# Optimization experiments

Measured on AMD Instinct MI355X. Metric: run time of the kernel, lower is better.

Reference implementation:

```python
import jax, jax.numpy as jnp
import numpy as np

N_NODES = 50000
N_EDGES = 1600000
N_GRAPHS = 64


def gcn_conv(x, edge_index, W, b):
    """GCNConv: out = D^{-1/2} (A + I) D^{-1/2} X W + b (symmetric norm, self-loops)."""
    n = x.shape[0]
    src = jnp.concatenate([edge_index[0], jnp.arange(n)])  # add self-loops
    dst = jnp.concatenate([edge_index[1], jnp.arange(n)])
    deg = jax.ops.segment_sum(jnp.ones_like(dst, dtype=x.dtype), dst, num_segments=n)
    dinv = jax.lax.rsqrt(jnp.maximum(deg, 1.0))
    norm = dinv[src] * dinv[dst]                      # [E+N]
    h = x @ W                                          # transform first (smaller gather)
    msg = norm[:, None] * h[src]                       # [E+N, out_dim]
    out = jax.ops.segment_sum(msg, dst, num_segments=n)
    return out + b


def global_mean_pool(x, batch, num_graphs):
    s = jax.ops.segment_sum(x, batch, num_segments=num_graphs)
    cnt = jax.ops.segment_sum(jnp.ones((x.shape[0],), x.dtype), batch, num_segments=num_graphs)
    return s / jnp.maximum(cnt, 1.0)[:, None]


def setup_inputs() -> dict:
    key = jax.random.key(0)
    ks = jax.random.split(key, 6)
    x = jax.random.normal(ks[0], (N_NODES, 256), dtype=jnp.float32)
    edge_index = jax.random.randint(ks[1], (2, N_EDGES), 0, N_NODES, dtype=jnp.int64)
    batch = jnp.sort(jax.random.randint(ks[2], (N_NODES,), 0, N_GRAPHS, dtype=jnp.int64))
    W1 = jax.random.normal(ks[3], (256, 256), dtype=jnp.float32) * (1.0 / np.sqrt(256))
    b1 = jnp.zeros((256,), jnp.float32)
    W2 = jax.random.normal(ks[4], (256, 10), dtype=jnp.float32) * (1.0 / np.sqrt(256))
    b2 = jnp.zeros((10,), jnp.float32)
    return {"x": x, "edge_index": edge_index, "batch": batch,
            "W1": W1, "b1": b1, "W2": W2, "b2": b2}


def reference(x, edge_index, batch, W1, b1, W2, b2):
    h = gcn_conv(x, edge_index, W1, b1)
    h = jax.nn.elu(h)
    # dropout: identity (inference mode, training=False)
    h = gcn_conv(h, edge_index, W2, b2)
    h = jax.nn.elu(h)
    g = global_mean_pool(h, batch, N_GRAPHS)          # [num_graphs, num_class]
    return jax.nn.log_softmax(g, axis=-1)
```

## Files before the change

kernel.cpp:

```cpp
#include <hip/hip_runtime.h>
#include <hip/hip_bf16.h>
#include <math.h>

typedef unsigned int uint;
typedef unsigned short ushort;

typedef __attribute__((ext_vector_type(8))) short bf16x8;
typedef __attribute__((ext_vector_type(4))) float f32x4;

#define SBLK_SHIFT 12
#define SBLK_STRIDE 16

__device__ __forceinline__ float bf2f_lo(uint u) {
    return __uint_as_float(u << 16);
}
__device__ __forceinline__ float bf2f_hi(uint u) {
    return __uint_as_float(u & 0xffff0000u);
}
__device__ __forceinline__ ushort f2bf(float f) {
    uint u = __float_as_uint(f);
    uint rounding = 0x7fffu + ((u >> 16) & 1u);
    return (ushort)((u + rounding) >> 16);
}
__device__ __forceinline__ float elu(float x) {
    return x > 0.f ? x : expm1f(x);
}

__global__ void count2_kernel(const int* __restrict__ src, const int* __restrict__ dst, int E,
                              int* __restrict__ cnt2) {
    int i = blockIdx.x * blockDim.x + threadIdx.x;
    int stride = gridDim.x * blockDim.x;
    for (; i < E; i += stride)
        atomicAdd(&cnt2[dst[i] * SBLK_STRIDE + (src[i] >> SBLK_SHIFT)], 1);
}

__global__ void scan1_kernel(const int* __restrict__ cnt, int M, int* __restrict__ partials) {
    __shared__ int sh[256];
    int i = blockIdx.x * 256 + threadIdx.x;
    sh[threadIdx.x] = (i < M) ? cnt[i] : 0;
    __syncthreads();
    for (int s = 128; s > 0; s >>= 1) {
        if (threadIdx.x < s) sh[threadIdx.x] += sh[threadIdx.x + s];
        __syncthreads();
    }
    if (threadIdx.x == 0) partials[blockIdx.x] = sh[0];
}

__global__ __launch_bounds__(256) void scan2_kernel(const int* __restrict__ partials, int nb,
                                                    int* __restrict__ pscan) {
    __shared__ int tsum[256];
    int t = threadIdx.x;
    int pref[16];
    int s = 0;
    #pragma unroll
    for (int j = 0; j < 16; ++j) {
        int idx = t * 16 + j;
        int v = (idx < nb) ? partials[idx] : 0;
        pref[j] = s;
        s += v;
    }
    tsum[t] = s;
    __syncthreads();
    for (int d = 1; d < 256; d <<= 1) {
        int x = (t >= d) ? tsum[t - d] : 0;
        __syncthreads();
        tsum[t] += x;
        __syncthreads();
    }
    int base = (t == 0) ? 0 : tsum[t - 1];
    #pragma unroll
    for (int j = 0; j < 16; ++j) {
        int idx = t * 16 + j;
        if (idx < nb) pscan[idx] = base + pref[j];
    }
}

__global__ void scan3_kernel(const int* __restrict__ cnt, int M, const int* __restrict__ pscan,
                             int* __restrict__ offs2, int* __restrict__ cursor2) {
    __shared__ int sh[256];
    int t = threadIdx.x;
    int i = blockIdx.x * 256 + t;
    int v = (i < M) ? cnt[i] : 0;
    sh[t] = v;
    __syncthreads();
    for (int d = 1; d < 256; d <<= 1) {
        int x = (t >= d) ? sh[t - d] : 0;
        __syncthreads();
        sh[t] += x;
        __syncthreads();
    }
    int excl = sh[t] - v;
    int base = pscan[blockIdx.x];
    if (i < M) {
        offs2[i]   = base + excl;
        cursor2[i] = base + excl;
    }
}

__global__ void post_kernel(const int* __restrict__ offs2, int NN, int E,
                            int* __restrict__ offs, float* __restrict__ dinv) {
    int n = blockIdx.x * blockDim.x + threadIdx.x;
    if (n >= NN) return;
    int o = offs2[n * SBLK_STRIDE];
    int nxt = (n == NN - 1) ? E : offs2[(n + 1) * SBLK_STRIDE];
    offs[n] = o;
    dinv[n] = rsqrtf((float)(nxt - o) + 1.0f);
    if (n == NN - 1) offs[NN] = E;
}

__global__ __launch_bounds__(256) void scatter_kernel(const int* __restrict__ src,
                                                      const int* __restrict__ dst, int E,
                                                      int* __restrict__ cursor2,
                                                      int* __restrict__ ssrc, int NN) {
    int grp = blockIdx.x & 7;
    int per = (NN + 7) >> 3;
    int lo = grp * per;
    int hi = min(NN, lo + per);
    int bid = blockIdx.x >> 3;
    int nb  = gridDim.x >> 3;
    int i = bid * blockDim.x + threadIdx.x;
    int stride = nb * blockDim.x;
    for (; i < E; i += stride) {
        int d = dst[i];
        if (d >= lo && d < hi) {
            int s = src[i];
            int pos = atomicAdd(&cursor2[d * SBLK_STRIDE + (s >> SBLK_SHIFT)], 1);
            ssrc[pos] = s;
        }
    }
}

__global__ void gstart_kernel(const int* __restrict__ batch, int NN, int NG,
                              int* __restrict__ gstart) {
    int g = blockIdx.x * blockDim.x + threadIdx.x;
    if (g > NG) return;
    int lo = 0, hi = NN;
    while (lo < hi) {
        int mid = (lo + hi) >> 1;
        if (batch[mid] < g) lo = mid + 1; else hi = mid;
    }
    gstart[g] = lo;
}

__global__ __launch_bounds__(256) void wtrans_kernel(const float* __restrict__ W,
                                                     ushort* __restrict__ WT) {
    __shared__ float T[64][68];
    int b = blockIdx.x;
    int kt = (b >> 2) * 64, nt = (b & 3) * 64;
    int t = threadIdx.x;
    int r = t >> 4, c4 = (t & 15) * 4;
    #pragma unroll
    for (int h = 0; h < 4; ++h) {
        int rr = r + h * 16;
        float4 v = *reinterpret_cast<const float4*>(&W[(size_t)(kt + rr) * 256 + nt + c4]);
        *reinterpret_cast<float4*>(&T[rr][c4]) = v;
    }
    __syncthreads();
    int nr = t >> 2, ks = (t & 3) * 16;
    uint o[8];
    #pragma unroll
    for (int i = 0; i < 16; i += 2) {
        float f0 = T[ks + i][nr];
        float f1 = T[ks + i + 1][nr];
        o[i >> 1] = (uint)f2bf(f0) | ((uint)f2bf(f1) << 16);
    }
    size_t base = (size_t)(nt + nr) * 256 + kt + ks;
    *reinterpret_cast<uint4*>(&WT[base])     = make_uint4(o[0], o[1], o[2], o[3]);
    *reinterpret_cast<uint4*>(&WT[base + 8]) = make_uint4(o[4], o[5], o[6], o[7]);
}

#define G1_STRIDE 40
__global__ __launch_bounds__(256) void gemm1_mfma_kernel(const float* __restrict__ X,
                                                         const ushort* __restrict__ W1T,
                                                         const float* __restrict__ dinv,
                                                         ushort* __restrict__ H1, int M) {
    __shared__ ushort Xs[64 * G1_STRIDE];
    __shared__ ushort Ws[256 * G1_STRIDE];
    __shared__ float  Dvs[64];
    int t = threadIdx.x;
    int row0 = blockIdx.x * 64;
    int lane = t & 63;
    int w = t >> 6;
    int lr = lane & 15;
    int lg = lane >> 4;

    if (t < 64) {
        int grow = row0 + t;
        Dvs[t] = (grow < M) ? dinv[grow] : 0.f;
    }

    f32x4 acc[4][4];
    #pragma unroll
    for (int j = 0; j < 4; ++j)
        #pragma unroll
        for (int i = 0; i < 4; ++i)
            acc[j][i] = (f32x4){0.f, 0.f, 0.f, 0.f};

    for (int k0 = 0; k0 < 256; k0 += 32) {
        #pragma unroll
        for (int h = 0; h < 2; ++h) {
            int u = t + h * 256;
            int row = u >> 3;
            int kq = (u & 7) * 4;
            int grow = row0 + row;
            float4 v = make_float4(0.f, 0.f, 0.f, 0.f);
            if (grow < M) v = *reinterpret_cast<const float4*>(&X[(size_t)grow * 256 + k0 + kq]);
            uint lo = (uint)f2bf(v.x) | ((uint)f2bf(v.y) << 16);
            uint hi = (uint)f2bf(v.z) | ((uint)f2bf(v.w) << 16);
            *reinterpret_cast<uint2*>(&Xs[row * G1_STRIDE + kq]) = make_uint2(lo, hi);
        }
        #pragma unroll
        for (int h = 0; h < 4; ++h) {
            int u = t + h * 256;
            int n = u >> 2;
            int seg = u & 3;
            uint4 wv = *reinterpret_cast<const uint4*>(&W1T[(size_t)n * 256 + k0 + seg * 8]);
            *reinterpret_cast<uint4*>(&Ws[n * G1_STRIDE + seg * 8]) = wv;
        }
        __syncthreads();
        bf16x8 wf[4], xf[4];
        #pragma unroll
        for (int j = 0; j < 4; ++j)
            wf[j] = *reinterpret_cast<const bf16x8*>(&Ws[(w * 64 + j * 16 + lr) * G1_STRIDE + lg * 8]);
        #pragma unroll
        for (int i = 0; i < 4; ++i)
            xf[i] = *reinterpret_cast<const bf16x8*>(&Xs[(i * 16 + lr) * G1_STRIDE + lg * 8]);
        #pragma unroll
        for (int j = 0; j < 4; ++j)
            #pragma unroll
            for (int i = 0; i < 4; ++i)
                acc[j][i] = __builtin_amdgcn_mfma_f32_16x16x32_bf16(wf[j], xf[i], acc[j][i], 0, 0, 0);
        __syncthreads();
    }

    #pragma unroll
    for (int mi = 0; mi < 4; ++mi) {
        int grow = row0 + mi * 16 + lr;
        float dv = Dvs[mi * 16 + lr];
        bool ok = grow < M;
        #pragma unroll
        for (int nj = 0; nj < 4; ++nj) {
            f32x4 a = acc[nj][mi];
            uint lo = (uint)f2bf(a[0] * dv) | ((uint)f2bf(a[1] * dv) << 16);
            uint hi = (uint)f2bf(a[2] * dv) | ((uint)f2bf(a[3] * dv) << 16);
            if (ok) {
                int col = w * 64 + nj * 16 + lg * 4;
                *reinterpret_cast<uint2*>(&H1[(size_t)grow * 256 + col]) = make_uint2(lo, hi);
            }
        }
    }
}

__global__ __launch_bounds__(256) void agg1_gemm2_kernel(
    const ushort* __restrict__ H1, const int* __restrict__ offs, const int* __restrict__ ssrc,
    const float* __restrict__ dinv, const float* __restrict__ b1, const float* __restrict__ W2,
    float* __restrict__ H2, int NN) {
    int lane = threadIdx.x & 63;
    int node = blockIdx.x * 4 + (threadIdx.x >> 6);
    if (node >= NN) return;
    int beg = offs[node], end = offs[node + 1];
    int col = lane * 4;
    const ushort* H1c = H1 + col;
    float acc0 = 0.f, acc1 = 0.f, acc2 = 0.f, acc3 = 0.f;
    int i = beg;
    for (; i + 3 < end; i += 4) {
        int s0 = ssrc[i], s1 = ssrc[i + 1], s2 = ssrc[i + 2], s3 = ssrc[i + 3];
        uint2 p0 = *reinterpret_cast<const uint2*>(H1c + (size_t)s0 * 256);
        uint2 p1 = *reinterpret_cast<const uint2*>(H1c + (size_t)s1 * 256);
        uint2 p2 = *reinterpret_cast<const uint2*>(H1c + (size_t)s2 * 256);
        uint2 p3 = *reinterpret_cast<const uint2*>(H1c + (size_t)s3 * 256);
        acc0 += bf2f_lo(p0.x) + bf2f_lo(p1.x) + bf2f_lo(p2.x) + bf2f_lo(p3.x);
        acc1 += bf2f_hi(p0.x) + bf2f_hi(p1.x) + bf2f_hi(p2.x) + bf2f_hi(p3.x);
        acc2 += bf2f_lo(p0.y) + bf2f_lo(p1.y) + bf2f_lo(p2.y) + bf2f_lo(p3.y);
        acc3 += bf2f_hi(p0.y) + bf2f_hi(p1.y) + bf2f_hi(p2.y) + bf2f_hi(p3.y);
    }
    for (; i < end; ++i) {
        int s = ssrc[i];
        uint2 p = *reinterpret_cast<const uint2*>(H1c + (size_t)s * 256);
        acc0 += bf2f_lo(p.x);
        acc1 += bf2f_hi(p.x);
        acc2 += bf2f_lo(p.y);
        acc3 += bf2f_hi(p.y);
    }
    {
        uint2 p = *reinterpret_cast<const uint2*>(H1c + (size_t)node * 256);
        acc0 += bf2f_lo(p.x);
        acc1 += bf2f_hi(p.x);
        acc2 += bf2f_lo(p.y);
        acc3 += bf2f_hi(p.y);
    }
    float dn = dinv[node];
    float a0 = elu(fmaf(acc0, dn, b1[col + 0]));
    float a1 = elu(fmaf(acc1, dn, b1[col + 1]));
    float a2 = elu(fmaf(acc2, dn, b1[col + 2]));
    float a3 = elu(fmaf(acc3, dn, b1[col + 3]));
    float hv = 0.f;
    #pragma unroll
    for (int c = 0; c < 10; ++c) {
        float p = a0 * W2[(col + 0) * 10 + c]
                + a1 * W2[(col + 1) * 10 + c]
                + a2 * W2[(col + 2) * 10 + c]
                + a3 * W2[(col + 3) * 10 + c];
        #pragma unroll
        for (int m = 1; m < 64; m <<= 1) p += __shfl_xor(p, m, 64);
        if (lane == c) hv = p;
    }
    if (lane < 10) H2[(size_t)node * 10 + lane] = dn * hv;
}

__global__ __launch_bounds__(256) void agg2_elu_kernel(
    const float* __restrict__ H2, const int* __restrict__ offs, const int* __restrict__ ssrc,
    const float* __restrict__ dinv, const float* __restrict__ b2,
    float* __restrict__ H2act, int NN) {
    int t = threadIdx.x;
    int node = blockIdx.x * 8 + (t >> 5);
    if (node >= NN) return;
    int sub = t & 31;
    int c = sub & 15;
    int e2 = sub >> 4;
    int beg = offs[node], end = offs[node + 1];
    float acc = 0.f;
    int i = beg + e2;
    for (; i + 6 < end; i += 8) {
        int s0 = ssrc[i], s1 = ssrc[i + 2], s2 = ssrc[i + 4], s3 = ssrc[i + 6];
        float h0 = H2[(size_t)s0 * 10 + c];
        float h1 = H2[(size_t)s1 * 10 + c];
        float h2 = H2[(size_t)s2 * 10 + c];
        float h3 = H2[(size_t)s3 * 10 + c];
        acc += (h0 + h1) + (h2 + h3);
    }
    for (; i < end; i += 2) acc += H2[(size_t)ssrc[i] * 10 + c];
    if (e2 == 0) acc += H2[(size_t)node * 10 + c];
    acc += __shfl_xor(acc, 16, 64);
    if (sub < 10) {
        float dn = dinv[node];
        H2act[(size_t)node * 10 + c] = elu(fmaf(dn, acc, b2[c]));
    }
}

__global__ __launch_bounds__(320) void pool_final_kernel(
    const float* __restrict__ H2act, const int* __restrict__ gstart,
    float* __restrict__ out, int NG) {
    __shared__ float red[32][10];
    __shared__ float m[10];
    __shared__ float s_lse;
    int g = blockIdx.x;
    int t = threadIdx.x;
    int grp = t / 10;
    int c = t - grp * 10;
    int lo = gstart[g], hi = gstart[g + 1];
    float acc = 0.f;
    if (grp < 32) {
        for (int n = lo + grp; n < hi; n += 32) acc += H2act[(size_t)n * 10 + c];
        red[grp][c] = acc;
    }
    __syncthreads();
    if (t < 10) {
        float s = 0.f;
        #pragma unroll
        for (int j = 0; j < 32; ++j) s += red[j][t];
        m[t] = s / fmaxf((float)(hi - lo), 1.0f);
    }
    __syncthreads();
    if (t == 0) {
        float mx = -1e30f;
        for (int c2 = 0; c2 < 10; ++c2) mx = fmaxf(mx, m[c2]);
        float s = 0.f;
        for (int c2 = 0; c2 < 10; ++c2) s += expf(m[c2] - mx);
        s_lse = logf(s) + mx;
    }
    __syncthreads();
    if (t < 10) out[g * 10 + t] = m[t] - s_lse;
}

extern "C" void kernel_launch(void* const* d_in, const int* in_sizes, int n_in,
                              void* d_out, int out_size, void* d_ws, size_t ws_size,
                              hipStream_t stream) {
    const float* x     = (const float*)d_in[0];
    const int*   eidx  = (const int*)d_in[1];
    const int*   batch = (const int*)d_in[2];
    const float* W1    = (const float*)d_in[3];
    const float* b1    = (const float*)d_in[4];
    const float* W2    = (const float*)d_in[5];
    const float* b2    = (const float*)d_in[6];

    int NN = in_sizes[0] / 256;
    int E  = in_sizes[1] / 2;
    int NG = out_size / 10;
    const int* src = eidx;
    const int* dst = eidx + E;

    int M2 = NN * SBLK_STRIDE;

    char* ws = (char*)d_ws;
    size_t off = 0;
    auto alloc = [&](size_t bytes) -> void* {
        void* p = ws + off;
        off += (bytes + 255) & ~((size_t)255);
        return p;
    };
    int*    cnt2     = (int*)alloc((size_t)M2 * 4);
    int*    offs2    = (int*)alloc((size_t)M2 * 4);
    int*    cursor2  = (int*)alloc((size_t)M2 * 4);
    int*    offs     = (int*)alloc((size_t)(NN + 1) * 4);
    int*    partials = (int*)alloc(4096 * 4);
    int*    pscan    = (int*)alloc(4096 * 4);
    float*  dinv     = (float*)alloc((size_t)NN * 4);
    int*    gstart   = (int*)alloc((size_t)(NG + 1) * 4);
    ushort* W1T      = (ushort*)alloc((size_t)256 * 256 * 2);
    int*    ssrc     = (int*)alloc((size_t)E * 4);
    ushort* H1       = (ushort*)alloc((size_t)NN * 256 * 2);
    float*  H2       = (float*)alloc((size_t)NN * 10 * 4);
    float*  H2act    = (float*)alloc((size_t)NN * 10 * 4);

    hipMemsetAsync(cnt2, 0, (size_t)M2 * 4, stream);

    int nb2 = (M2 + 255) / 256;
    count2_kernel <<<1024, 256, 0, stream>>>(src, dst, E, cnt2);
    scan1_kernel  <<<nb2, 256, 0, stream>>>(cnt2, M2, partials);
    scan2_kernel  <<<1, 256, 0, stream>>>(partials, nb2, pscan);
    scan3_kernel  <<<nb2, 256, 0, stream>>>(cnt2, M2, pscan, offs2, cursor2);
    post_kernel   <<<(NN + 255) / 256, 256, 0, stream>>>(offs2, NN, E, offs, dinv);
    scatter_kernel<<<2048, 256, 0, stream>>>(src, dst, E, cursor2, ssrc, NN);
    gstart_kernel <<<1, 128, 0, stream>>>(batch, NN, NG, gstart);
    wtrans_kernel <<<16, 256, 0, stream>>>(W1, W1T);
    gemm1_mfma_kernel<<<(NN + 63) / 64, 256, 0, stream>>>(x, W1T, dinv, H1, NN);
    agg1_gemm2_kernel<<<(NN + 3) / 4, 256, 0, stream>>>(H1, offs, ssrc, dinv, b1, W2, H2, NN);
    agg2_elu_kernel  <<<(NN + 7) / 8, 256, 0, stream>>>(H2, offs, ssrc, dinv, b2, H2act, NN);
    pool_final_kernel<<<NG, 320, 0, stream>>>(H2act, gstart, (float*)d_out, NG);
}
```

Baseline: 337.4 us.

## Store layer-1 features in FP8 and pad layer-2 features to 16 columns

The GEMM1 output H1 is now stored as FP8 (e4m3 via the packed convert builtins) instead of bf16, which halves the bytes gathered per edge in the layer-1 aggregation. The aggregation unpacks each 4-byte word with the hardware FP8-to-f32 conversions. H2 rows are also padded from 10 to 16 floats so the per-edge gathers in the layer-2 aggregation are aligned. The risk is a large loss of precision in the layer-1 activations, which could push the output outside tolerance.

Result: faster. 308.7 us (-8.5%).

```diff
diff --git a/kernel.cpp b/kernel.cpp
--- a/kernel.cpp
+++ b/kernel.cpp
@@ -4,19 +4,16 @@
 
 typedef unsigned int uint;
 typedef unsigned short ushort;
+typedef unsigned char uchar;
 
 typedef __attribute__((ext_vector_type(8))) short bf16x8;
 typedef __attribute__((ext_vector_type(4))) float f32x4;
+typedef __attribute__((ext_vector_type(2))) float f32x2;
 
 #define SBLK_SHIFT 12
 #define SBLK_STRIDE 16
-
-__device__ __forceinline__ float bf2f_lo(uint u) {
-    return __uint_as_float(u << 16);
-}
-__device__ __forceinline__ float bf2f_hi(uint u) {
-    return __uint_as_float(u & 0xffff0000u);
-}
+#define H2S 16
+
 __device__ __forceinline__ ushort f2bf(float f) {
     uint u = __float_as_uint(f);
     uint rounding = 0x7fffu + ((u >> 16) & 1u);
@@ -173,7 +170,7 @@
 __global__ __launch_bounds__(256) void gemm1_mfma_kernel(const float* __restrict__ X,
                                                          const ushort* __restrict__ W1T,
                                                          const float* __restrict__ dinv,
-                                                         ushort* __restrict__ H1, int M) {
+                                                         uchar* __restrict__ H1, int M) {
     __shared__ ushort Xs[64 * G1_STRIDE];
     __shared__ ushort Ws[256 * G1_STRIDE];
     __shared__ float  Dvs[64];
@@ -241,18 +238,18 @@
         #pragma unroll
         for (int nj = 0; nj < 4; ++nj) {
             f32x4 a = acc[nj][mi];
-            uint lo = (uint)f2bf(a[0] * dv) | ((uint)f2bf(a[1] * dv) << 16);
-            uint hi = (uint)f2bf(a[2] * dv) | ((uint)f2bf(a[3] * dv) << 16);
+            int pk = __builtin_amdgcn_cvt_pk_fp8_f32(a[0] * dv, a[1] * dv, 0, false);
+            pk     = __builtin_amdgcn_cvt_pk_fp8_f32(a[2] * dv, a[3] * dv, pk, true);
             if (ok) {
                 int col = w * 64 + nj * 16 + lg * 4;
-                *reinterpret_cast<uint2*>(&H1[(size_t)grow * 256 + col]) = make_uint2(lo, hi);
+                *reinterpret_cast<uint*>(&H1[(size_t)grow * 256 + col]) = (uint)pk;
             }
         }
     }
 }
 
 __global__ __launch_bounds__(256) void agg1_gemm2_kernel(
-    const ushort* __restrict__ H1, const int* __restrict__ offs, const int* __restrict__ ssrc,
+    const uchar* __restrict__ H1, const int* __restrict__ offs, const int* __restrict__ ssrc,
     const float* __restrict__ dinv, const float* __restrict__ b1, const float* __restrict__ W2,
     float* __restrict__ H2, int NN) {
     int lane = threadIdx.x & 63;
@@ -260,34 +257,40 @@
     if (node >= NN) return;
     int beg = offs[node], end = offs[node + 1];
     int col = lane * 4;
-    const ushort* H1c = H1 + col;
+    const uchar* H1c = H1 + col;
     float acc0 = 0.f, acc1 = 0.f, acc2 = 0.f, acc3 = 0.f;
     int i = beg;
     for (; i + 3 < end; i += 4) {
         int s0 = ssrc[i], s1 = ssrc[i + 1], s2 = ssrc[i + 2], s3 = ssrc[i + 3];
-        uint2 p0 = *reinterpret_cast<const uint2*>(H1c + (size_t)s0 * 256);
-        uint2 p1 = *reinterpret_cast<const uint2*>(H1c + (size_t)s1 * 256);
-        uint2 p2 = *reinterpret_cast<const uint2*>(H1c + (size_t)s2 * 256);
-        uint2 p3 = *reinterpret_cast<const uint2*>(H1c + (size_t)s3 * 256);
-        acc0 += bf2f_lo(p0.x) + bf2f_lo(p1.x) + bf2f_lo(p2.x) + bf2f_lo(p3.x);
-        acc1 += bf2f_hi(p0.x) + bf2f_hi(p1.x) + bf2f_hi(p2.x) + bf2f_hi(p3.x);
-        acc2 += bf2f_lo(p0.y) + bf2f_lo(p1.y) + bf2f_lo(p2.y) + bf2f_lo(p3.y);
-        acc3 += bf2f_hi(p0.y) + bf2f_hi(p1.y) + bf2f_hi(p2.y) + bf2f_hi(p3.y);
+        uint p0 = *reinterpret_cast<const uint*>(H1c + (size_t)s0 * 256);
+        uint p1 = *reinterpret_cast<const uint*>(H1c + (size_t)s1 * 256);
+        uint p2 = *reinterpret_cast<const uint*>(H1c + (size_t)s2 * 256);
+        uint p3 = *reinterpret_cast<const uint*>(H1c + (size_t)s3 * 256);
+        f32x2 l0 = __builtin_amdgcn_cvt_pk_f32_fp8((int)p0, false);
+        f32x2 h0 = __builtin_amdgcn_cvt_pk_f32_fp8((int)p0, true);
+        f32x2 l1 = __builtin_amdgcn_cvt_pk_f32_fp8((int)p1, false);
+        f32x2 h1 = __builtin_amdgcn_cvt_pk_f32_fp8((int)p1, true);
+        f32x2 l2 = __builtin_amdgcn_cvt_pk_f32_fp8((int)p2, false);
+        f32x2 h2 = __builtin_amdgcn_cvt_pk_f32_fp8((int)p2, true);
+        f32x2 l3 = __builtin_amdgcn_cvt_pk_f32_fp8((int)p3, false);
+        f32x2 h3 = __builtin_amdgcn_cvt_pk_f32_fp8((int)p3, true);
+        acc0 += (l0.x + l1.x) + (l2.x + l3.x);
+        acc1 += (l0.y + l1.y) + (l2.y + l3.y);
+        acc2 += (h0.x + h1.x) + (h2.x + h3.x);
+        acc3 += (h0.y + h1.y) + (h2.y + h3.y);
     }
     for (; i < end; ++i) {
         int s = ssrc[i];
-        uint2 p = *reinterpret_cast<const uint2*>(H1c + (size_t)s * 256);
-        acc0 += bf2f_lo(p.x);
-        acc1 += bf2f_hi(p.x);
-        acc2 += bf2f_lo(p.y);
-        acc3 += bf2f_hi(p.y);
+        uint p = *reinterpret_cast<const uint*>(H1c + (size_t)s * 256);
+        f32x2 l = __builtin_amdgcn_cvt_pk_f32_fp8((int)p, false);
+        f32x2 h = __builtin_amdgcn_cvt_pk_f32_fp8((int)p, true);
+        acc0 += l.x; acc1 += l.y; acc2 += h.x; acc3 += h.y;
     }
     {
-        uint2 p = *reinterpret_cast<const uint2*>(H1c + (size_t)node * 256);
-        acc0 += bf2f_lo(p.x);
-        acc1 += bf2f_hi(p.x);
-        acc2 += bf2f_lo(p.y);
-        acc3 += bf2f_hi(p.y);
+        uint p = *reinterpret_cast<const uint*>(H1c + (size_t)node * 256);
+        f32x2 l = __builtin_amdgcn_cvt_pk_f32_fp8((int)p, false);
+        f32x2 h = __builtin_amdgcn_cvt_pk_f32_fp8((int)p, true);
+        acc0 += l.x; acc1 += l.y; acc2 += h.x; acc3 += h.y;
     }
     float dn = dinv[node];
     float a0 = elu(fmaf(acc0, dn, b1[col + 0]));
@@ -305,7 +308,7 @@
         for (int m = 1; m < 64; m <<= 1) p += __shfl_xor(p, m, 64);
         if (lane == c) hv = p;
     }
-    if (lane < 10) H2[(size_t)node * 10 + lane] = dn * hv;
+    if (lane < 10) H2[(size_t)node * H2S + lane] = dn * hv;
 }
 
 __global__ __launch_bounds__(256) void agg2_elu_kernel(
@@ -323,14 +326,14 @@
     int i = beg + e2;
     for (; i + 6 < end; i += 8) {
         int s0 = ssrc[i], s1 = ssrc[i + 2], s2 = ssrc[i + 4], s3 = ssrc[i + 6];
-        float h0 = H2[(size_t)s0 * 10 + c];
-        float h1 = H2[(size_t)s1 * 10 + c];
-        float h2 = H2[(size_t)s2 * 10 + c];
-        float h3 = H2[(size_t)s3 * 10 + c];
+        float h0 = H2[(size_t)s0 * H2S + c];
+        float h1 = H2[(size_t)s1 * H2S + c];
+        float h2 = H2[(size_t)s2 * H2S + c];
+        float h3 = H2[(size_t)s3 * H2S + c];
         acc += (h0 + h1) + (h2 + h3);
     }
-    for (; i < end; i += 2) acc += H2[(size_t)ssrc[i] * 10 + c];
-    if (e2 == 0) acc += H2[(size_t)node * 10 + c];
+    for (; i < end; i += 2) acc += H2[(size_t)ssrc[i] * H2S + c];
+    if (e2 == 0) acc += H2[(size_t)node * H2S + c];
     acc += __shfl_xor(acc, 16, 64);
     if (sub < 10) {
         float dn = dinv[node];
@@ -409,8 +412,8 @@
     int*    gstart   = (int*)alloc((size_t)(NG + 1) * 4);
     ushort* W1T      = (ushort*)alloc((size_t)256 * 256 * 2);
     int*    ssrc     = (int*)alloc((size_t)E * 4);
-    ushort* H1       = (ushort*)alloc((size_t)NN * 256 * 2);
-    float*  H2       = (float*)alloc((size_t)NN * 10 * 4);
+    uchar*  H1       = (uchar*)alloc((size_t)NN * 256);
+    float*  H2       = (float*)alloc((size_t)NN * H2S * 4);
     float*  H2act    = (float*)alloc((size_t)NN * 10 * 4);
 
     hipMemsetAsync(cnt2, 0, (size_t)M2 * 4, stream);
```
